# Optimization experiments

Hardware: AMD Instinct MI355X
Metric: run time of the kernel (lower is better)

The kernel has to match this reference:

```python
import jax, jax.numpy as jnp
import numpy as np

N = 50000
E = 800000
IN_DIM = 256
HID_DIM = 256
OUT_DIM = 128


def _gcn(x, src, dst, W, b):
    # PyG GCNConv: h = W x; add self-loops; sym-normalized scatter-add; + bias
    h = x @ W  # [N, out]
    deg = jax.ops.segment_sum(jnp.ones_like(dst, dtype=h.dtype), dst, num_segments=N)
    dinv = jax.lax.rsqrt(jnp.maximum(deg, 1e-12))
    norm = dinv[src] * dinv[dst]  # [E+N]
    msg = h[src] * norm[:, None]  # gather + scale
    out = jax.ops.segment_sum(msg, dst, num_segments=N)  # scatter-add
    return out + b


def _with_self_loops(edge):
    loops = jnp.arange(N, dtype=edge.dtype)
    src = jnp.concatenate([edge[0], loops])
    dst = jnp.concatenate([edge[1], loops])
    return src, dst


def setup_inputs() -> dict:
    key = jax.random.key(0)
    ks = jax.random.split(key, 20)
    d = {}
    d['x'] = jax.random.normal(ks[0], (N, IN_DIM), dtype=jnp.float32)
    d['edge_ppi'] = jax.random.randint(ks[1], (2, E), 0, N, dtype=jnp.int32)
    d['edge_path'] = jax.random.randint(ks[2], (2, E), 0, N, dtype=jnp.int32)
    d['edge_go'] = jax.random.randint(ks[3], (2, E), 0, N, dtype=jnp.int32)
    i = 4
    for name in ['ppi', 'path', 'go']:
        s1 = 1.0 / np.sqrt(IN_DIM)
        s2 = 1.0 / np.sqrt(HID_DIM)
        d[f'{name}_w1'] = jax.random.uniform(ks[i], (IN_DIM, HID_DIM), jnp.float32, -s1, s1); i += 1
        d[f'{name}_b1'] = jnp.zeros((HID_DIM,), jnp.float32)
        d[f'{name}_w2'] = jax.random.uniform(ks[i], (HID_DIM, OUT_DIM), jnp.float32, -s2, s2); i += 1
        d[f'{name}_b2'] = jnp.zeros((OUT_DIM,), jnp.float32)
    sa = 1.0 / np.sqrt(OUT_DIM)
    d['attn_w'] = jax.random.uniform(ks[i], (OUT_DIM, 1), jnp.float32, -sa, sa)
    d['attn_b'] = jnp.zeros((1,), jnp.float32)
    return d


def reference(x, edge_ppi, edge_path, edge_go,
              ppi_w1, ppi_b1, ppi_w2, ppi_b2,
              path_w1, path_b1, path_w2, path_b2,
              go_w1, go_b1, go_w2, go_b2,
              attn_w, attn_b):
    feats = []
    for edge, w1, b1, w2, b2 in [
        (edge_ppi, ppi_w1, ppi_b1, ppi_w2, ppi_b2),
        (edge_path, path_w1, path_b1, path_w2, path_b2),
        (edge_go, go_w1, go_b1, go_w2, go_b2),
    ]:
        src, dst = _with_self_loops(edge)
        h = jax.nn.relu(_gcn(x, src, dst, w1, b1))
        feats.append(_gcn(h, src, dst, w2, b2))
    all_feat = jnp.stack(feats, axis=1)  # [N, 3, out]
    attn = jax.nn.softmax(all_feat @ attn_w + attn_b, axis=1)  # [N, 3, 1]
    return jnp.sum(all_feat * attn, axis=1)  # [N, out]
```

## Files before the change

kernel.cpp:

```cpp
#include <hip/hip_runtime.h>

#define NN 50000
#define NE 800000
#define BINS 98
#define CAP 12288
#define EPB 4096
#define P1B ((NE + EPB - 1) / EPB)

typedef __attribute__((ext_vector_type(8))) short short8;
typedef __attribute__((ext_vector_type(4))) float f32x4;
typedef __attribute__((ext_vector_type(8))) unsigned short ushort8v;
typedef __attribute__((ext_vector_type(4))) unsigned short ushort4v;
typedef _Float16 half8 __attribute__((ext_vector_type(8)));

__device__ __forceinline__ ushort f2bf(float f) {
    unsigned u = __float_as_uint(f);
    unsigned r = (u + 0x7fffu + ((u >> 16) & 1u)) >> 16;
    return (ushort)r;
}
__device__ __forceinline__ float bf2f(ushort h) {
    return __uint_as_float(((unsigned)h) << 16);
}
__device__ __forceinline__ ushort f2h(float f) {
    _Float16 h = (_Float16)f;
    return __builtin_bit_cast(ushort, h);
}
__device__ __forceinline__ float h2f(ushort u) {
    return (float)__builtin_bit_cast(_Float16, u);
}


__global__ __launch_bounds__(256) void k_bin(const int* __restrict__ e0,
                                             const int* __restrict__ e1,
                                             const int* __restrict__ e2,
                                             int* __restrict__ g_cur,
                                             unsigned* __restrict__ g_bins) {
    const int br = blockIdx.x / P1B;
    const int cb = blockIdx.x % P1B;
    const int* ep = (br == 0 ? e0 : br == 1 ? e1 : e2);
    const int tid = threadIdx.x;
    const int e_base = cb * EPB;

    __shared__ int s_cnt[BINS];
    __shared__ int s_start[BINS];
    __shared__ int s_cur[BINS];
    __shared__ int s_gb[BINS];
    __shared__ unsigned s_stage[EPB];

    if (tid < BINS) s_cnt[tid] = 0;
    __syncthreads();

    int4 s4[4], d4[4];
    bool valid[4];
#pragma unroll
    for (int i = 0; i < 4; ++i) {
        int idx = e_base + i * 1024 + tid * 4;
        valid[i] = (idx < NE);
        if (valid[i]) {
            s4[i] = *(const int4*)&ep[idx];
            d4[i] = *(const int4*)&ep[NE + idx];
            atomicAdd(&s_cnt[d4[i].x >> 9], 1);
            atomicAdd(&s_cnt[d4[i].y >> 9], 1);
            atomicAdd(&s_cnt[d4[i].z >> 9], 1);
            atomicAdd(&s_cnt[d4[i].w >> 9], 1);
        }
    }
    __syncthreads();
    if (tid == 0) {
        int run = 0;
        for (int b = 0; b < BINS; ++b) {
            s_start[b] = run;
            run += s_cnt[b];
        }
    }
    __syncthreads();
    if (tid < BINS) {
        s_cur[tid] = s_start[tid];
        int c = s_cnt[tid];
        int pc = (c + 15) & ~15;
        s_gb[tid] = (c > 0) ? atomicAdd(&g_cur[br * BINS + tid], pc) : 0;
    }
    __syncthreads();

#pragma unroll
    for (int i = 0; i < 4; ++i) {
        if (valid[i]) {
            int ss[4] = {s4[i].x, s4[i].y, s4[i].z, s4[i].w};
            int dd[4] = {d4[i].x, d4[i].y, d4[i].z, d4[i].w};
#pragma unroll
            for (int q = 0; q < 4; ++q) {
                int bin = dd[q] >> 9;
                int pos = atomicAdd(&s_cur[bin], 1);
                s_stage[pos] = ((unsigned)(dd[q] & 511) << 16) | (unsigned)ss[q];
            }
        }
    }
    __syncthreads();

    for (int b = 0; b < BINS; ++b) {
        int c = s_cnt[b];
        if (c == 0) continue;
        int st = s_start[b];
        int gb = s_gb[b];
        int pc = (c + 15) & ~15;
        if (gb + pc > CAP) pc = (gb < CAP) ? (CAP - gb) : 0;
        size_t obase = (size_t)(br * BINS + b) * CAP + gb;
        for (int j = tid; j < pc; j += 256)
            g_bins[obase + j] = (j < c) ? s_stage[st + j] : 0x80000000u;
    }
}


__device__ __forceinline__ int wave_incl_scan(int v, int lane) {
#pragma unroll
    for (int d = 1; d < 64; d <<= 1) {
        int u = __shfl_up(v, d);
        if (lane >= d) v += u;
    }
    return v;
}

__global__ __launch_bounds__(256) void k_build(const unsigned* __restrict__ g_bins,
                                               const int* __restrict__ g_cur,
                                               ushort* __restrict__ g_csr,
                                               int* __restrict__ seg3,
                                               int* __restrict__ cnt3,
                                               float* __restrict__ dinv3) {
    const int bid = blockIdx.x;
    const int br = bid / BINS;
    const int b2 = bid % BINS;
    const size_t base = (size_t)bid * CAP;
    const int node0 = b2 << 9;
    const int tid = threadIdx.x;

    __shared__ int s_cnt[512];
    __shared__ int s_off[512];
    __shared__ int s_wsum[4];

    s_cnt[tid] = 0;
    s_cnt[tid + 256] = 0;
    __syncthreads();

    const int total = min(g_cur[bid], CAP);
    for (int j = tid; j < total; j += 256) {
        unsigned p = g_bins[base + j];
        if (!(p & 0x80000000u)) atomicAdd(&s_cnt[(p >> 16) & 0x1FF], 1);
    }
    __syncthreads();

    const int lane = tid & 63, w = tid >> 6;
    int c0 = s_cnt[2 * tid], c1 = s_cnt[2 * tid + 1];
    int c2 = c0 + c1;
    int incl = wave_incl_scan(c2, lane);
    if (lane == 63) s_wsum[w] = incl;
    __syncthreads();
    int wpre = 0;
    for (int i = 0; i < w; ++i) wpre += s_wsum[i];
    int ex = wpre + incl - c2;
    s_off[2 * tid] = ex;
    s_off[2 * tid + 1] = ex + c0;

#pragma unroll
    for (int q = 0; q < 2; ++q) {
        int local = 2 * tid + q;
        int node = node0 + local;
        if (node < NN) {
            int g = br * NN + node;
            int c = (q == 0) ? c0 : c1;
            seg3[g] = (int)base + s_off[local];
            cnt3[g] = c;
            dinv3[g] = rsqrtf((float)(c + 1));
        }
    }
    __syncthreads();
    s_cnt[2 * tid] = s_off[2 * tid];
    s_cnt[2 * tid + 1] = s_off[2 * tid + 1];
    __syncthreads();

    for (int j = tid; j < total; j += 256) {
        unsigned p = g_bins[base + j];
        if (!(p & 0x80000000u)) {
            int loc = (p >> 16) & 0x1FF;
            int pos = atomicAdd(&s_cnt[loc], 1);
            g_csr[base + pos] = (ushort)(p & 0xFFFFu);
        }
    }
}


__global__ __launch_bounds__(256) void k_conv_x(const float* __restrict__ x,
                                                ushort* __restrict__ xp) {
    const int wid = threadIdx.x >> 6, lane = threadIdx.x & 63;
    const int row = blockIdx.x * 4 + wid;
    if (row >= NN) return;
    float4 v = *(const float4*)&x[(size_t)row * 256 + lane * 4];
    ushort4 hi, lo;
    hi.x = f2bf(v.x); lo.x = f2bf(v.x - bf2f(hi.x));
    hi.y = f2bf(v.y); lo.y = f2bf(v.y - bf2f(hi.y));
    hi.z = f2bf(v.z); lo.z = f2bf(v.z - bf2f(hi.z));
    hi.w = f2bf(v.w); lo.w = f2bf(v.w - bf2f(hi.w));
    *(ushort4*)&xp[(size_t)row * 512 + lane * 4] = hi;
    *(ushort4*)&xp[(size_t)row * 512 + 256 + lane * 4] = lo;
}

__global__ __launch_bounds__(256) void k_conv_w1(const float* __restrict__ w0,
                                                 const float* __restrict__ w1,
                                                 const float* __restrict__ w2,
                                                 ushort* __restrict__ BT1all) {
    int idx = blockIdx.x * 256 + threadIdx.x;
    int b = idx >> 16, r = idx & 65535;
    int k = r >> 8, n = r & 255;
    const float* W = (b == 0 ? w0 : b == 1 ? w1 : w2);
    float w = W[r];
    ushort hi = f2bf(w);
    ushort lo = f2bf(w - bf2f(hi));
    ushort* row = BT1all + (size_t)b * 196608 + (size_t)n * 768;
    row[k] = hi;
    row[256 + k] = hi;
    row[512 + k] = lo;
}

__global__ __launch_bounds__(256) void k_conv_w2(const float* __restrict__ w0,
                                                 const float* __restrict__ w1,
                                                 const float* __restrict__ w2,
                                                 ushort* __restrict__ BT2all) {
    int idx = blockIdx.x * 256 + threadIdx.x;
    int b = idx >> 15, r = idx & 32767;
    int k = r >> 7, n = r & 127;
    const float* W = (b == 0 ? w0 : b == 1 ? w1 : w2);
    BT2all[(size_t)b * 32768 + (size_t)n * 256 + k] = f2h(W[r]);
}


template <int BM, int BN, int N, int KK, int AK, bool HALF>
__global__ __launch_bounds__((BM / 64) * (BN / 64) * 64) void k_gemm(
    const ushort* __restrict__ A, size_t aBatch,
    const ushort* __restrict__ BTall, int btBatch,
    const float* __restrict__ dinv3, ushort* __restrict__ Call, size_t cBatch) {
    constexpr int WGN = BN / 64, NW = (BM / 64) * WGN;
    constexpr int BK = 32;
    constexpr int MT = (NN + BM - 1) / BM, NT = N / BN, GB = MT * NT;
    constexpr int NSTEP = KK / BK;
    __shared__ ushort sA[2][BM * BK];
    __shared__ ushort sB[2][BN * BK];
    const int kb = blockIdx.x / GB;
    const int bid = blockIdx.x % GB;
    const ushort* Ab = A + (size_t)kb * aBatch;
    const ushort* BT = BTall + (size_t)kb * btBatch;
    const float* dinv = dinv3 + (size_t)kb * NN;
    ushort* C = Call + (size_t)kb * cBatch;
    const int t = threadIdx.x, lane = t & 63, wid = t >> 6;
    const int wm = (wid / WGN) * 64, wn = (wid % WGN) * 64;
    const int bm = (bid / NT) * BM;
    const int bn = (bid % NT) * BN;

    f32x4 zero = {0.f, 0.f, 0.f, 0.f};
    f32x4 acc[4][4];
#pragma unroll
    for (int m = 0; m < 4; ++m)
#pragma unroll
        for (int n = 0; n < 4; ++n) acc[m][n] = zero;

    constexpr int A_ISS = (BM * BK * 2) / (NW * 1024);
    constexpr int B_ISS = (BN * BK * 2) / (NW * 1024);

    auto stage = [&](int buf, int kt) {
        const int akt = (kt >= AK) ? kt - AK : kt;
#pragma unroll
        for (int i = 0; i < A_ISS; ++i) {
            int off = (wid + i * NW) << 10;
            int la = off + lane * 16;
            int row = la >> 6;
            int slot = (la >> 4) & 3;
            int scol = (slot ^ (row & 3)) << 4;
            int grow = bm + row;
            if (grow > NN - 1) grow = NN - 1;
            const char* ga = (const char*)Ab + (size_t)grow * (AK * 2) + akt * 2 + scol;
            __builtin_amdgcn_global_load_lds(
                (__attribute__((address_space(1))) const void*)ga,
                (__attribute__((address_space(3))) void*)((char*)sA[buf] + off), 16, 0, 0);
        }
#pragma unroll
        for (int i = 0; i < B_ISS; ++i) {
            int off = (wid + i * NW) << 10;
            int la = off + lane * 16;
            int row = la >> 6;
            int slot = (la >> 4) & 3;
            int scol = (slot ^ (row & 3)) << 4;
            const char* ga = (const char*)BT + (size_t)(bn + row) * (KK * 2) + kt * 2 + scol;
            __builtin_amdgcn_global_load_lds(
                (__attribute__((address_space(1))) const void*)ga,
                (__attribute__((address_space(3))) void*)((char*)sB[buf] + off), 16, 0, 0);
        }
    };

    stage(0, 0);
    __syncthreads();

    int cur = 0;
    for (int ts = 0; ts < NSTEP; ++ts) {
        if (ts + 1 < NSTEP) stage(cur ^ 1, (ts + 1) * BK);

        const int s = lane >> 4;
        const int r0 = lane & 15;
        short8 af[4], bf[4];
#pragma unroll
        for (int m = 0; m < 4; ++m) {
            int row = wm + m * 16 + r0;
            af[m] = *(const short8*)((const char*)sA[cur] + row * 64 + ((s ^ (row & 3)) << 4));
        }
#pragma unroll
        for (int n = 0; n < 4; ++n) {
            int row = wn + n * 16 + r0;
            bf[n] = *(const short8*)((const char*)sB[cur] + row * 64 + ((s ^ (row & 3)) << 4));
        }
#pragma unroll
        for (int m = 0; m < 4; ++m)
#pragma unroll
            for (int n = 0; n < 4; ++n) {
                if constexpr (HALF)
                    acc[m][n] = __builtin_amdgcn_mfma_f32_16x16x32_f16(
                        __builtin_bit_cast(half8, af[m]), __builtin_bit_cast(half8, bf[n]),
                        acc[m][n], 0, 0, 0);
                else
                    acc[m][n] = __builtin_amdgcn_mfma_f32_16x16x32_bf16(af[m], bf[n],
                                                                        acc[m][n], 0, 0, 0);
            }
        __syncthreads();
        cur ^= 1;
    }

    const int cr0 = (lane >> 4) * 4;
    const int cc = lane & 15;
#pragma unroll
    for (int m = 0; m < 4; ++m) {
#pragma unroll
        for (int r = 0; r < 4; ++r) {
            int row = bm + wm + m * 16 + cr0 + r;
            if (row < NN) {
                float dv = dinv[row];
#pragma unroll
                for (int n = 0; n < 4; ++n)
                    C[(size_t)row * N + bn + wn + n * 16 + cc] = f2h(acc[m][n][r] * dv);
            }
        }
    }
}


__global__ __launch_bounds__(256) void k_agg1(const ushort* __restrict__ hs16all,
                                              const int* __restrict__ seg3,
                                              const int* __restrict__ cnt3,
                                              const ushort* __restrict__ g_csr,
                                              const float* __restrict__ dinv3,
                                              const float* __restrict__ b1a,
                                              const float* __restrict__ b1b,
                                              const float* __restrict__ b1c,
                                              ushort* __restrict__ h1all) {
    constexpr int WBn = (NN + 3) / 4;
    const int b = blockIdx.x / WBn;
    const int blk = blockIdx.x % WBn;
    const int wid = threadIdx.x >> 6;
    const int lane = threadIdx.x & 63;
    const int node = blk * 4 + wid;
    if (node >= NN) return;
    const int half = lane >> 5, l32 = lane & 31;
    const int g = b * NN + node;
    const ushort* hs = hs16all + (size_t)b * NN * 256;
    const ushort* csr = g_csr + seg3[g];
    const int len = cnt3[g] + 1;
    const size_t colb = (size_t)l32 * 8;

    float acc[8] = {0.f, 0.f, 0.f, 0.f, 0.f, 0.f, 0.f, 0.f};
    int i = half;
    for (; i + 6 < len; i += 8) {
        int s0 = (i == 0) ? node : (int)csr[i - 1];
        int s1 = (int)csr[i + 1];
        int s2 = (int)csr[i + 3];
        int s3 = (int)csr[i + 5];
        ushort8v v0 = *(const ushort8v*)&hs[(size_t)s0 * 256 + colb];
        ushort8v v1 = *(const ushort8v*)&hs[(size_t)s1 * 256 + colb];
        ushort8v v2 = *(const ushort8v*)&hs[(size_t)s2 * 256 + colb];
        ushort8v v3 = *(const ushort8v*)&hs[(size_t)s3 * 256 + colb];
#pragma unroll
        for (int j = 0; j < 8; ++j)
            acc[j] += (h2f(v0[j]) + h2f(v1[j])) + (h2f(v2[j]) + h2f(v3[j]));
    }
    for (; i < len; i += 2) {
        int s = (i == 0) ? node : (int)csr[i - 1];
        ushort8v v = *(const ushort8v*)&hs[(size_t)s * 256 + colb];
#pragma unroll
        for (int j = 0; j < 8; ++j) acc[j] += h2f(v[j]);
    }
#pragma unroll
    for (int j = 0; j < 8; ++j) acc[j] += __shfl_xor(acc[j], 32);

    if (half == 0) {
        const float* bias = (b == 0 ? b1a : b == 1 ? b1b : b1c);
        const float di = dinv3[g];
        ushort8v o;
#pragma unroll
        for (int j = 0; j < 8; ++j) {
            float r = fmaxf(di * acc[j] + bias[l32 * 8 + j], 0.f);
            o[j] = f2h(r);
        }
        *(ushort8v*)&h1all[((size_t)b * NN + node) * 256 + colb] = o;
    }
}


__global__ __launch_bounds__(256) void k_final(const ushort* __restrict__ hs2all,
                                               const int* __restrict__ seg3,
                                               const int* __restrict__ cnt3,
                                               const ushort* __restrict__ g_csr,
                                               const float* __restrict__ dinv3,
                                               const float* __restrict__ b2a,
                                               const float* __restrict__ b2b,
                                               const float* __restrict__ b2c,
                                               const float* __restrict__ attn_w,
                                               const float* __restrict__ attn_b,
                                               float* __restrict__ out) {
    const int wid = threadIdx.x >> 6;
    const int lane = threadIdx.x & 63;
    const int node = blockIdx.x * 4 + wid;
    if (node >= NN) return;
    const int half = lane >> 5, l32 = lane & 31;
    const size_t colb = (size_t)l32 * 4;

    float f[3][4];
#pragma unroll
    for (int b = 0; b < 3; ++b) {
        const int g = b * NN + node;
        const ushort* hs = hs2all + (size_t)b * NN * 128;
        const ushort* csr = g_csr + seg3[g];
        const int len = cnt3[g] + 1;
        float acc[4] = {0.f, 0.f, 0.f, 0.f};
        int i = half;
        for (; i + 6 < len; i += 8) {
            int s0 = (i == 0) ? node : (int)csr[i - 1];
            int s1 = (int)csr[i + 1];
            int s2 = (int)csr[i + 3];
            int s3 = (int)csr[i + 5];
            ushort4v v0 = *(const ushort4v*)&hs[(size_t)s0 * 128 + colb];
            ushort4v v1 = *(const ushort4v*)&hs[(size_t)s1 * 128 + colb];
            ushort4v v2 = *(const ushort4v*)&hs[(size_t)s2 * 128 + colb];
            ushort4v v3 = *(const ushort4v*)&hs[(size_t)s3 * 128 + colb];
#pragma unroll
            for (int j = 0; j < 4; ++j)
                acc[j] += (h2f(v0[j]) + h2f(v1[j])) + (h2f(v2[j]) + h2f(v3[j]));
        }
        for (; i < len; i += 2) {
            int s = (i == 0) ? node : (int)csr[i - 1];
            ushort4v v = *(const ushort4v*)&hs[(size_t)s * 128 + colb];
#pragma unroll
            for (int j = 0; j < 4; ++j) acc[j] += h2f(v[j]);
        }
#pragma unroll
        for (int j = 0; j < 4; ++j) acc[j] += __shfl_xor(acc[j], 32);
        const float* bias = (b == 0 ? b2a : b == 1 ? b2b : b2c);
        const float di = dinv3[g];
#pragma unroll
        for (int j = 0; j < 4; ++j) f[b][j] = di * acc[j] + bias[l32 * 4 + j];
    }

    float4 w = *(const float4*)&attn_w[l32 * 4];
    float s0 = f[0][0] * w.x + f[0][1] * w.y + f[0][2] * w.z + f[0][3] * w.w;
    float s1 = f[1][0] * w.x + f[1][1] * w.y + f[1][2] * w.z + f[1][3] * w.w;
    float s2 = f[2][0] * w.x + f[2][1] * w.y + f[2][2] * w.z + f[2][3] * w.w;
#pragma unroll
    for (int m = 16; m >= 1; m >>= 1) {
        s0 += __shfl_xor(s0, m);
        s1 += __shfl_xor(s1, m);
        s2 += __shfl_xor(s2, m);
    }
    float bb = attn_b[0];
    s0 += bb; s1 += bb; s2 += bb;
    float mx = fmaxf(s0, fmaxf(s1, s2));
    float e0 = expf(s0 - mx), e1 = expf(s1 - mx), e2 = expf(s2 - mx);
    float inv = 1.f / (e0 + e1 + e2);
    e0 *= inv; e1 *= inv; e2 *= inv;

    if (half == 0) {
        float4 o;
        o.x = f[0][0] * e0 + f[1][0] * e1 + f[2][0] * e2;
        o.y = f[0][1] * e0 + f[1][1] * e1 + f[2][1] * e2;
        o.z = f[0][2] * e0 + f[1][2] * e1 + f[2][2] * e2;
        o.w = f[0][3] * e0 + f[1][3] * e1 + f[2][3] * e2;
        *(float4*)&out[(size_t)node * 128 + colb] = o;
    }
}


extern "C" void kernel_launch(void* const* d_in, const int* in_sizes, int n_in,
                              void* d_out, int out_size, void* d_ws, size_t ws_size,
                              hipStream_t stream) {
    const float* x = (const float*)d_in[0];
    const int* e0 = (const int*)d_in[1];
    const int* e1 = (const int*)d_in[2];
    const int* e2 = (const int*)d_in[3];
    const float* attn_w = (const float*)d_in[16];
    const float* attn_b = (const float*)d_in[17];

    char* ws = (char*)d_ws;
    size_t off = 0;
    auto alloc = [&](size_t bytes) -> void* {
        void* p = ws + off;
        off += (bytes + 255) & ~(size_t)255;
        return p;
    };

    int* g_cur      = (int*)alloc(3 * BINS * 4);
    int* seg3       = (int*)alloc((size_t)3 * NN * 4);
    int* cnt3       = (int*)alloc((size_t)3 * NN * 4);
    float* dinv3    = (float*)alloc((size_t)3 * NN * 4);
    ushort* g_csr   = (ushort*)alloc((size_t)3 * BINS * CAP * 2);
    ushort* xp      = (ushort*)alloc((size_t)NN * 512 * 2);
    ushort* hs2all  = xp;
    ushort* hs16all = (ushort*)alloc((size_t)3 * NN * 256 * 2);
    ushort* h1all   = (ushort*)alloc((size_t)3 * NN * 256 * 2);
    unsigned* g_bins = (unsigned*)h1all;
    ushort* BT1all  = (ushort*)alloc((size_t)3 * 256 * 768 * 2);
    ushort* BT2all  = (ushort*)alloc((size_t)3 * 128 * 256 * 2);

    const int WB = (NN + 3) / 4;

    hipMemsetAsync(g_cur, 0, 3 * BINS * 4, stream);
    k_conv_x<<<WB, 256, 0, stream>>>(x, xp);
    k_conv_w1<<<768, 256, 0, stream>>>((const float*)d_in[4], (const float*)d_in[8],
                                       (const float*)d_in[12], BT1all);
    k_conv_w2<<<384, 256, 0, stream>>>((const float*)d_in[6], (const float*)d_in[10],
                                       (const float*)d_in[14], BT2all);

    k_bin<<<3 * P1B, 256, 0, stream>>>(e0, e1, e2, g_cur, g_bins);
    k_build<<<3 * BINS, 256, 0, stream>>>(g_bins, g_cur, g_csr, seg3, cnt3, dinv3);

    k_gemm<128, 256, 256, 768, 512, false><<<3 * 391, 512, 0, stream>>>(
        xp, 0, BT1all, 196608, dinv3, hs16all, (size_t)NN * 256);
    k_agg1<<<3 * WB, 256, 0, stream>>>(hs16all, seg3, cnt3, g_csr, dinv3,
                                       (const float*)d_in[5], (const float*)d_in[9],
                                       (const float*)d_in[13], h1all);

    k_gemm<128, 128, 128, 256, 256, true><<<3 * 391, 256, 0, stream>>>(
        h1all, (size_t)NN * 256, BT2all, 32768, dinv3, hs2all, (size_t)NN * 128);

    k_final<<<WB, 256, 0, stream>>>(hs2all, seg3, cnt3, g_csr, dinv3,
                                    (const float*)d_in[7], (const float*)d_in[11],
                                    (const float*)d_in[15], attn_w, attn_b,
                                    (float*)d_out);
}
```

Baseline: 483.2 us.

## Aggregate raw features before layer-1 GEMM and fuse both GEMMs per row tile

Reorders layer 1 as A·(XW) = (AX)·W. The fp16-converted input x is aggregated over the graph first, with per-source normalisation and a split bf16 hi/lo output, and the result feeds a single kernel that runs the layer-1 GEMM, adds bias and ReLU, keeps the hidden tile in shared memory, and then runs the layer-2 GEMM from it directly. This removes the hidden-activation round trip through global memory and one kernel launch. In exchange, x is now aggregated in fp16, which changes precision, and the layer-2 weights are read from global memory without staging in shared memory.

```diff
diff --git a/kernel.cpp b/kernel.cpp
--- a/kernel.cpp
+++ b/kernel.cpp
@@ -188,19 +188,15 @@
 }
 
 
-__global__ __launch_bounds__(256) void k_conv_x(const float* __restrict__ x,
-                                                ushort* __restrict__ xp) {
+__global__ __launch_bounds__(256) void k_conv_x16(const float* __restrict__ x,
+                                                  ushort* __restrict__ x16) {
     const int wid = threadIdx.x >> 6, lane = threadIdx.x & 63;
     const int row = blockIdx.x * 4 + wid;
     if (row >= NN) return;
     float4 v = *(const float4*)&x[(size_t)row * 256 + lane * 4];
-    ushort4 hi, lo;
-    hi.x = f2bf(v.x); lo.x = f2bf(v.x - bf2f(hi.x));
-    hi.y = f2bf(v.y); lo.y = f2bf(v.y - bf2f(hi.y));
-    hi.z = f2bf(v.z); lo.z = f2bf(v.z - bf2f(hi.z));
-    hi.w = f2bf(v.w); lo.w = f2bf(v.w - bf2f(hi.w));
-    *(ushort4*)&xp[(size_t)row * 512 + lane * 4] = hi;
-    *(ushort4*)&xp[(size_t)row * 512 + 256 + lane * 4] = lo;
+    ushort4 o;
+    o.x = f2h(v.x); o.y = f2h(v.y); o.z = f2h(v.z); o.w = f2h(v.w);
+    *(ushort4*)&x16[(size_t)row * 256 + lane * 4] = o;
 }
 
 __global__ __launch_bounds__(256) void k_conv_w1(const float* __restrict__ w0,
@@ -232,141 +228,21 @@
 }
 
 
-template <int BM, int BN, int N, int KK, int AK, bool HALF>
-__global__ __launch_bounds__((BM / 64) * (BN / 64) * 64) void k_gemm(
-    const ushort* __restrict__ A, size_t aBatch,
-    const ushort* __restrict__ BTall, int btBatch,
-    const float* __restrict__ dinv3, ushort* __restrict__ Call, size_t cBatch) {
-    constexpr int WGN = BN / 64, NW = (BM / 64) * WGN;
-    constexpr int BK = 32;
-    constexpr int MT = (NN + BM - 1) / BM, NT = N / BN, GB = MT * NT;
-    constexpr int NSTEP = KK / BK;
-    __shared__ ushort sA[2][BM * BK];
-    __shared__ ushort sB[2][BN * BK];
-    const int kb = blockIdx.x / GB;
-    const int bid = blockIdx.x % GB;
-    const ushort* Ab = A + (size_t)kb * aBatch;
-    const ushort* BT = BTall + (size_t)kb * btBatch;
-    const float* dinv = dinv3 + (size_t)kb * NN;
-    ushort* C = Call + (size_t)kb * cBatch;
-    const int t = threadIdx.x, lane = t & 63, wid = t >> 6;
-    const int wm = (wid / WGN) * 64, wn = (wid % WGN) * 64;
-    const int bm = (bid / NT) * BM;
-    const int bn = (bid % NT) * BN;
-
-    f32x4 zero = {0.f, 0.f, 0.f, 0.f};
-    f32x4 acc[4][4];
-#pragma unroll
-    for (int m = 0; m < 4; ++m)
-#pragma unroll
-        for (int n = 0; n < 4; ++n) acc[m][n] = zero;
-
-    constexpr int A_ISS = (BM * BK * 2) / (NW * 1024);
-    constexpr int B_ISS = (BN * BK * 2) / (NW * 1024);
-
-    auto stage = [&](int buf, int kt) {
-        const int akt = (kt >= AK) ? kt - AK : kt;
-#pragma unroll
-        for (int i = 0; i < A_ISS; ++i) {
-            int off = (wid + i * NW) << 10;
-            int la = off + lane * 16;
-            int row = la >> 6;
-            int slot = (la >> 4) & 3;
-            int scol = (slot ^ (row & 3)) << 4;
-            int grow = bm + row;
-            if (grow > NN - 1) grow = NN - 1;
-            const char* ga = (const char*)Ab + (size_t)grow * (AK * 2) + akt * 2 + scol;
-            __builtin_amdgcn_global_load_lds(
-                (__attribute__((address_space(1))) const void*)ga,
-                (__attribute__((address_space(3))) void*)((char*)sA[buf] + off), 16, 0, 0);
-        }
-#pragma unroll
-        for (int i = 0; i < B_ISS; ++i) {
-            int off = (wid + i * NW) << 10;
-            int la = off + lane * 16;
-            int row = la >> 6;
-            int slot = (la >> 4) & 3;
-            int scol = (slot ^ (row & 3)) << 4;
-            const char* ga = (const char*)BT + (size_t)(bn + row) * (KK * 2) + kt * 2 + scol;
-            __builtin_amdgcn_global_load_lds(
-                (__attribute__((address_space(1))) const void*)ga,
-                (__attribute__((address_space(3))) void*)((char*)sB[buf] + off), 16, 0, 0);
-        }
-    };
-
-    stage(0, 0);
-    __syncthreads();
-
-    int cur = 0;
-    for (int ts = 0; ts < NSTEP; ++ts) {
-        if (ts + 1 < NSTEP) stage(cur ^ 1, (ts + 1) * BK);
-
-        const int s = lane >> 4;
-        const int r0 = lane & 15;
-        short8 af[4], bf[4];
-#pragma unroll
-        for (int m = 0; m < 4; ++m) {
-            int row = wm + m * 16 + r0;
-            af[m] = *(const short8*)((const char*)sA[cur] + row * 64 + ((s ^ (row & 3)) << 4));
-        }
-#pragma unroll
-        for (int n = 0; n < 4; ++n) {
-            int row = wn + n * 16 + r0;
-            bf[n] = *(const short8*)((const char*)sB[cur] + row * 64 + ((s ^ (row & 3)) << 4));
-        }
-#pragma unroll
-        for (int m = 0; m < 4; ++m)
-#pragma unroll
-            for (int n = 0; n < 4; ++n) {
-                if constexpr (HALF)
-                    acc[m][n] = __builtin_amdgcn_mfma_f32_16x16x32_f16(
-                        __builtin_bit_cast(half8, af[m]), __builtin_bit_cast(half8, bf[n]),
-                        acc[m][n], 0, 0, 0);
-                else
-                    acc[m][n] = __builtin_amdgcn_mfma_f32_16x16x32_bf16(af[m], bf[n],
-                                                                        acc[m][n], 0, 0, 0);
-            }
-        __syncthreads();
-        cur ^= 1;
-    }
-
-    const int cr0 = (lane >> 4) * 4;
-    const int cc = lane & 15;
-#pragma unroll
-    for (int m = 0; m < 4; ++m) {
-#pragma unroll
-        for (int r = 0; r < 4; ++r) {
-            int row = bm + wm + m * 16 + cr0 + r;
-            if (row < NN) {
-                float dv = dinv[row];
-#pragma unroll
-                for (int n = 0; n < 4; ++n)
-                    C[(size_t)row * N + bn + wn + n * 16 + cc] = f2h(acc[m][n][r] * dv);
-            }
-        }
-    }
-}
-
-
-__global__ __launch_bounds__(256) void k_agg1(const ushort* __restrict__ hs16all,
+__global__ __launch_bounds__(256) void k_aggx(const ushort* __restrict__ x16,
                                               const int* __restrict__ seg3,
                                               const int* __restrict__ cnt3,
                                               const ushort* __restrict__ g_csr,
                                               const float* __restrict__ dinv3,
-                                              const float* __restrict__ b1a,
-                                              const float* __restrict__ b1b,
-                                              const float* __restrict__ b1c,
-                                              ushort* __restrict__ h1all) {
+                                              ushort* __restrict__ aggXp) {
     constexpr int WBn = (NN + 3) / 4;
     const int b = blockIdx.x / WBn;
     const int blk = blockIdx.x % WBn;
     const int wid = threadIdx.x >> 6;
     const int lane = threadIdx.x & 63;
     const int node = blk * 4 + wid;
-    if (node >= NN) return;
     const int half = lane >> 5, l32 = lane & 31;
     const int g = b * NN + node;
-    const ushort* hs = hs16all + (size_t)b * NN * 256;
+    const float* dv = dinv3 + (size_t)b * NN;
     const ushort* csr = g_csr + seg3[g];
     const int len = cnt3[g] + 1;
     const size_t colb = (size_t)l32 * 8;
@@ -378,33 +254,183 @@
         int s1 = (int)csr[i + 1];
         int s2 = (int)csr[i + 3];
         int s3 = (int)csr[i + 5];
-        ushort8v v0 = *(const ushort8v*)&hs[(size_t)s0 * 256 + colb];
-        ushort8v v1 = *(const ushort8v*)&hs[(size_t)s1 * 256 + colb];
-        ushort8v v2 = *(const ushort8v*)&hs[(size_t)s2 * 256 + colb];
-        ushort8v v3 = *(const ushort8v*)&hs[(size_t)s3 * 256 + colb];
+        float d0 = dv[s0], d1 = dv[s1], d2 = dv[s2], d3 = dv[s3];
+        ushort8v v0 = *(const ushort8v*)&x16[(size_t)s0 * 256 + colb];
+        ushort8v v1 = *(const ushort8v*)&x16[(size_t)s1 * 256 + colb];
+        ushort8v v2 = *(const ushort8v*)&x16[(size_t)s2 * 256 + colb];
+        ushort8v v3 = *(const ushort8v*)&x16[(size_t)s3 * 256 + colb];
 #pragma unroll
         for (int j = 0; j < 8; ++j)
-            acc[j] += (h2f(v0[j]) + h2f(v1[j])) + (h2f(v2[j]) + h2f(v3[j]));
+            acc[j] += (d0 * h2f(v0[j]) + d1 * h2f(v1[j])) +
+                      (d2 * h2f(v2[j]) + d3 * h2f(v3[j]));
     }
     for (; i < len; i += 2) {
         int s = (i == 0) ? node : (int)csr[i - 1];
-        ushort8v v = *(const ushort8v*)&hs[(size_t)s * 256 + colb];
-#pragma unroll
-        for (int j = 0; j < 8; ++j) acc[j] += h2f(v[j]);
+        float d = dv[s];
+        ushort8v v = *(const ushort8v*)&x16[(size_t)s * 256 + colb];
+#pragma unroll
+        for (int j = 0; j < 8; ++j) acc[j] += d * h2f(v[j]);
     }
 #pragma unroll
     for (int j = 0; j < 8; ++j) acc[j] += __shfl_xor(acc[j], 32);
 
+    const float di = dv[node];
+    ushort8v o;
     if (half == 0) {
-        const float* bias = (b == 0 ? b1a : b == 1 ? b1b : b1c);
-        const float di = dinv3[g];
-        ushort8v o;
+#pragma unroll
+        for (int j = 0; j < 8; ++j) o[j] = f2bf(di * acc[j]);
+        *(ushort8v*)&aggXp[(size_t)g * 512 + colb] = o;
+    } else {
 #pragma unroll
         for (int j = 0; j < 8; ++j) {
-            float r = fmaxf(di * acc[j] + bias[l32 * 8 + j], 0.f);
-            o[j] = f2h(r);
-        }
-        *(ushort8v*)&h1all[((size_t)b * NN + node) * 256 + colb] = o;
+            float v = di * acc[j];
+            ushort hi = f2bf(v);
+            o[j] = f2bf(v - bf2f(hi));
+        }
+        *(ushort8v*)&aggXp[(size_t)g * 512 + 256 + colb] = o;
+    }
+}
+
+
+__global__ __launch_bounds__(512) void k_gemm12(
+    const ushort* __restrict__ aggXp, const ushort* __restrict__ BT1all,
+    const ushort* __restrict__ BT2all, const float* __restrict__ dinv3,
+    const float* __restrict__ b1a, const float* __restrict__ b1b,
+    const float* __restrict__ b1c, ushort* __restrict__ hs2all) {
+    constexpr int BM = 128, BN = 256, KK = 768, AK = 512, BK = 32;
+    constexpr int MT = (NN + BM - 1) / BM;
+    constexpr int NW = 8, WGN = 4;
+    constexpr int NSTEP = KK / BK;
+
+    __shared__ char smem[65536];
+    const int kb = blockIdx.x / MT;
+    const int bid = blockIdx.x % MT;
+    const ushort* Ab = aggXp + (size_t)kb * NN * 512;
+    const ushort* BT = BT1all + (size_t)kb * 196608;
+    const int t = threadIdx.x, lane = t & 63, wid = t >> 6;
+    const int wm = (wid / WGN) * 64, wn = (wid % WGN) * 64;
+    const int bm = bid * BM;
+
+    f32x4 zero = {0.f, 0.f, 0.f, 0.f};
+    f32x4 acc[4][4];
+#pragma unroll
+    for (int m = 0; m < 4; ++m)
+#pragma unroll
+        for (int n = 0; n < 4; ++n) acc[m][n] = zero;
+
+    auto stage = [&](int buf, int kt) {
+        const int akt = (kt >= AK) ? kt - AK : kt;
+        {
+            int off = wid << 10;
+            int la = off + lane * 16;
+            int row = la >> 6;
+            int slot = (la >> 4) & 3;
+            int scol = (slot ^ (row & 3)) << 4;
+            int grow = bm + row;
+            if (grow > NN - 1) grow = NN - 1;
+            const char* ga = (const char*)Ab + (size_t)grow * 1024 + akt * 2 + scol;
+            __builtin_amdgcn_global_load_lds(
+                (__attribute__((address_space(1))) const void*)ga,
+                (__attribute__((address_space(3))) void*)(smem + buf * 8192 + off),
+                16, 0, 0);
+        }
+#pragma unroll
+        for (int i = 0; i < 2; ++i) {
+            int off = (wid + i * NW) << 10;
+            int la = off + lane * 16;
+            int row = la >> 6;
+            int slot = (la >> 4) & 3;
+            int scol = (slot ^ (row & 3)) << 4;
+            const char* ga = (const char*)BT + (size_t)row * (KK * 2) + kt * 2 + scol;
+            __builtin_amdgcn_global_load_lds(
+                (__attribute__((address_space(1))) const void*)ga,
+                (__attribute__((address_space(3))) void*)(smem + 16384 + buf * 16384 + off),
+                16, 0, 0);
+        }
+    };
+
+    stage(0, 0);
+    __syncthreads();
+
+    int cur = 0;
+    for (int ts = 0; ts < NSTEP; ++ts) {
+        if (ts + 1 < NSTEP) stage(cur ^ 1, (ts + 1) * BK);
+
+        const char* sA = smem + cur * 8192;
+        const char* sB = smem + 16384 + cur * 16384;
+        const int s = lane >> 4;
+        const int r0 = lane & 15;
+        short8 af[4], bf[4];
+#pragma unroll
+        for (int m = 0; m < 4; ++m) {
+            int row = wm + m * 16 + r0;
+            af[m] = *(const short8*)(sA + row * 64 + ((s ^ (row & 3)) << 4));
+        }
+#pragma unroll
+        for (int n = 0; n < 4; ++n) {
+            int row = wn + n * 16 + r0;
+            bf[n] = *(const short8*)(sB + row * 64 + ((s ^ (row & 3)) << 4));
+        }
+#pragma unroll
+        for (int m = 0; m < 4; ++m)
+#pragma unroll
+            for (int n = 0; n < 4; ++n)
+                acc[m][n] = __builtin_amdgcn_mfma_f32_16x16x32_bf16(af[m], bf[n],
+                                                                    acc[m][n], 0, 0, 0);
+        __syncthreads();
+        cur ^= 1;
+    }
+
+    const float* b1 = (kb == 0 ? b1a : kb == 1 ? b1b : b1c);
+    const int cr0 = (lane >> 4) * 4;
+    const int cc = lane & 15;
+#pragma unroll
+    for (int m = 0; m < 4; ++m) {
+#pragma unroll
+        for (int n = 0; n < 4; ++n) {
+            int col = wn + n * 16 + cc;
+            float bc = b1[col];
+#pragma unroll
+            for (int rg = 0; rg < 4; ++rg) {
+                int row = wm + m * 16 + cr0 + rg;
+                float v = fmaxf(acc[m][n][rg] + bc, 0.f);
+                *(ushort*)(smem + row * 512 + (((col >> 3) ^ (row & 31)) << 4) +
+                           (col & 7) * 2) = f2h(v);
+            }
+        }
+    }
+    __syncthreads();
+
+    const ushort* BT2 = BT2all + (size_t)kb * 32768;
+    const int r0 = lane & 15, s = lane >> 4;
+    f32x4 acc2[8];
+#pragma unroll
+    for (int n = 0; n < 8; ++n) acc2[n] = zero;
+#pragma unroll
+    for (int ks = 0; ks < 8; ++ks) {
+        const int kt = ks * 32;
+        const int arow = wid * 16 + r0;
+        short8 a = *(const short8*)(smem + arow * 512 +
+                                    ((((kt >> 3) + s) ^ (arow & 31)) << 4));
+#pragma unroll
+        for (int n = 0; n < 8; ++n) {
+            short8 bfr = *(const short8*)&BT2[(size_t)(n * 16 + r0) * 256 + kt + s * 8];
+            acc2[n] = __builtin_amdgcn_mfma_f32_16x16x32_f16(
+                __builtin_bit_cast(half8, a), __builtin_bit_cast(half8, bfr),
+                acc2[n], 0, 0, 0);
+        }
+    }
+
+#pragma unroll
+    for (int rg = 0; rg < 4; ++rg) {
+        int node = bm + wid * 16 + cr0 + rg;
+        if (node < NN) {
+            float dvv = dinv3[(size_t)kb * NN + node];
+            ushort* orow = hs2all + ((size_t)kb * NN + node) * 128;
+#pragma unroll
+            for (int n = 0; n < 8; ++n)
+                orow[n * 16 + cc] = f2h(acc2[n][rg] * dvv);
+        }
     }
 }
 
@@ -514,18 +540,17 @@
     int* cnt3       = (int*)alloc((size_t)3 * NN * 4);
     float* dinv3    = (float*)alloc((size_t)3 * NN * 4);
     ushort* g_csr   = (ushort*)alloc((size_t)3 * BINS * CAP * 2);
-    ushort* xp      = (ushort*)alloc((size_t)NN * 512 * 2);
-    ushort* hs2all  = xp;
-    ushort* hs16all = (ushort*)alloc((size_t)3 * NN * 256 * 2);
-    ushort* h1all   = (ushort*)alloc((size_t)3 * NN * 256 * 2);
-    unsigned* g_bins = (unsigned*)h1all;
+    ushort* x16     = (ushort*)alloc((size_t)NN * 256 * 2);
+    ushort* aggXp   = (ushort*)alloc((size_t)3 * NN * 512 * 2);
+    unsigned* g_bins = (unsigned*)aggXp;
+    ushort* hs2all  = (ushort*)alloc((size_t)3 * NN * 128 * 2);
     ushort* BT1all  = (ushort*)alloc((size_t)3 * 256 * 768 * 2);
     ushort* BT2all  = (ushort*)alloc((size_t)3 * 128 * 256 * 2);
 
     const int WB = (NN + 3) / 4;
 
     hipMemsetAsync(g_cur, 0, 3 * BINS * 4, stream);
-    k_conv_x<<<WB, 256, 0, stream>>>(x, xp);
+    k_conv_x16<<<WB, 256, 0, stream>>>(x, x16);
     k_conv_w1<<<768, 256, 0, stream>>>((const float*)d_in[4], (const float*)d_in[8],
                                        (const float*)d_in[12], BT1all);
     k_conv_w2<<<384, 256, 0, stream>>>((const float*)d_in[6], (const float*)d_in[10],
@@ -534,14 +559,12 @@
     k_bin<<<3 * P1B, 256, 0, stream>>>(e0, e1, e2, g_cur, g_bins);
     k_build<<<3 * BINS, 256, 0, stream>>>(g_bins, g_cur, g_csr, seg3, cnt3, dinv3);
 
-    k_gemm<128, 256, 256, 768, 512, false><<<3 * 391, 512, 0, stream>>>(
-        xp, 0, BT1all, 196608, dinv3, hs16all, (size_t)NN * 256);
-    k_agg1<<<3 * WB, 256, 0, stream>>>(hs16all, seg3, cnt3, g_csr, dinv3,
-                                       (const float*)d_in[5], (const float*)d_in[9],
-                                       (const float*)d_in[13], h1all);
-
-    k_gemm<128, 128, 128, 256, 256, true><<<3 * 391, 256, 0, stream>>>(
-        h1all, (size_t)NN * 256, BT2all, 32768, dinv3, hs2all, (size_t)NN * 128);
+    k_aggx<<<3 * WB, 256, 0, stream>>>(x16, seg3, cnt3, g_csr, dinv3, aggXp);
+
+    k_gemm12<<<3 * 391, 512, 0, stream>>>(
+        aggXp, BT1all, BT2all, dinv3,
+        (const float*)d_in[5], (const float*)d_in[9], (const float*)d_in[13],
+        hs2all);
 
     k_final<<<WB, 256, 0, stream>>>(hs2all, seg3, cnt3, g_csr, dinv3,
                                     (const float*)d_in[7], (const float*)d_in[11],
```

New measurement: 518.4 us. 7.3% more time.
